# Optimization experiments

Measured on AMD Instinct MI355X. Metric: run time of the kernel, lower is better.

The kernel has to match this reference:

```python
import jax, jax.numpy as jnp
import numpy as np

VOCAB, EMB, B, L, H, OUT = 100000, 300, 2048, 200, 128, 20

def setup_inputs() -> dict:
    key = jax.random.key(0)
    ks = jax.random.split(key, 7)
    x = jax.random.randint(ks[0], (B, L), 0, VOCAB, dtype=jnp.int64 if jax.config.read('jax_enable_x64') else jnp.int32)
    lengths = jax.random.randint(ks[1], (B,), 1, L + 1, dtype=x.dtype)  # avoid zero length
    emb_table = jax.random.normal(ks[2], (VOCAB, EMB), dtype=jnp.float32)
    W1 = jax.random.normal(ks[3], (EMB, H), dtype=jnp.float32) * (1.0 / np.sqrt(EMB))
    b1 = jax.random.normal(ks[4], (H,), dtype=jnp.float32) * 0.01
    W2 = jax.random.normal(ks[5], (H, OUT), dtype=jnp.float32) * (1.0 / np.sqrt(H))
    b2 = jax.random.normal(ks[6], (OUT,), dtype=jnp.float32) * 0.01
    return {"x": x, "lengths": lengths, "emb_table": emb_table,
            "W1": W1, "b1": b1, "W2": W2, "b2": b2}

def reference(x, lengths, emb_table, W1, b1, W2, b2):
    # embedding lookup: [B, L, EMB]
    emb = emb_table[x]
    # faithful to original: sum over FULL sequence, divide by per-sample length
    rep = emb.sum(axis=1) / lengths.astype(emb.dtype)[:, None]  # [B, EMB]
    h = jax.nn.relu(rep @ W1 + b1)                              # [B, H]
    logits = h @ W2 + b2                                        # [B, OUT]
    return logits
```

## Files before the change

kernel.cpp:

```cpp
#include <hip/hip_runtime.h>

typedef _Float16 f16;
typedef _Float16 f16x8 __attribute__((ext_vector_type(8)));
typedef float    f32x4 __attribute__((ext_vector_type(4)));

#define VOCAB 100000
#define BB   2048
#define LL   200
#define EMB  300
#define HH   128
#define OUTD 20
#define NSRT 256
#define RPW  50

#define KPAD 320

__global__ void w1t_prep(const float* __restrict__ W1,
                         f16* __restrict__ w1t_hi,
                         f16* __restrict__ w1t_lo)
{
    const int n = blockIdx.x;
    const int k = threadIdx.x;
    const float v = (k < EMB) ? W1[(size_t)k * HH + n] : 0.f;
    const f16 hi = (f16)v;
    const f16 lo = (f16)(v - (float)hi);
    w1t_hi[(size_t)n * KPAD + k] = hi;
    w1t_lo[(size_t)n * KPAD + k] = lo;
}

#define BMp 128
#define BKp 32
#define KSTEPS 10

__global__ __launch_bounds__(256, 3) void proj_mfma(
    const float* __restrict__ table,
    const f16*   __restrict__ w1t_hi,
    const f16*   __restrict__ w1t_lo,
    f16*         __restrict__ P)
{
    __shared__ f16 Af_hi[8][64][8];
    __shared__ f16 Af_lo[8][64][8];
    __shared__ f16 Bf_hi[8][64][8];
    __shared__ f16 Bf_lo[8][64][8];

    const int t    = threadIdx.x;
    const int w    = t >> 6;
    const int lane = t & 63;
    const int row0 = blockIdx.x * BMp;

    f32x4 acc[2][8];
    #pragma unroll
    for (int i = 0; i < 2; ++i)
        #pragma unroll
        for (int j = 0; j < 8; ++j) acc[i][j] = (f32x4)0.f;

    for (int ks = 0; ks < KSTEPS; ++ks) {
        const int k0 = ks * BKp;

        #pragma unroll
        for (int half = 0; half < 2; ++half) {
            const int e  = t + 256 * half;
            const int mt = e >> 6;
            const int l  = e & 63;
            const int m  = (mt << 4) + (l & 15);
            const int kg = l >> 4;
            const int row = row0 + m;
            const int k   = k0 + kg * 8;
            const float* src = table + (size_t)row * EMB + k;
            float4 v0 = make_float4(0.f, 0.f, 0.f, 0.f);
            float4 v1 = make_float4(0.f, 0.f, 0.f, 0.f);
            if (row < VOCAB && k + 4 <= EMB) v0 = *(const float4*)(src);
            if (row < VOCAB && k + 8 <= EMB) v1 = *(const float4*)(src + 4);
            const float vv[8] = {v0.x, v0.y, v0.z, v0.w, v1.x, v1.y, v1.z, v1.w};
            f16x8 hi, lo;
            #pragma unroll
            for (int j = 0; j < 8; ++j) {
                const f16 h = (f16)vv[j];
                hi[j] = h;
                lo[j] = (f16)(vv[j] - (float)h);
            }
            *(f16x8*)&Af_hi[mt][l][0] = hi;
            *(f16x8*)&Af_lo[mt][l][0] = lo;
        }

        #pragma unroll
        for (int half = 0; half < 2; ++half) {
            const int e  = t + 256 * half;
            const int nt = e >> 6;
            const int l  = e & 63;
            const int n  = (nt << 4) + (l & 15);
            const int kg = l >> 4;
            const size_t off = (size_t)n * KPAD + k0 + kg * 8;
            *(f16x8*)&Bf_hi[nt][l][0] = *(const f16x8*)(w1t_hi + off);
            *(f16x8*)&Bf_lo[nt][l][0] = *(const f16x8*)(w1t_lo + off);
        }
        __syncthreads();

        f16x8 a_hi[2], a_lo[2];
        #pragma unroll
        for (int mt2 = 0; mt2 < 2; ++mt2) {
            a_hi[mt2] = *(const f16x8*)&Af_hi[2 * w + mt2][lane][0];
            a_lo[mt2] = *(const f16x8*)&Af_lo[2 * w + mt2][lane][0];
        }
        #pragma unroll
        for (int h = 0; h < 2; ++h) {
            f16x8 b_hi[4], b_lo[4];
            #pragma unroll
            for (int n4 = 0; n4 < 4; ++n4) {
                const int nt = h * 4 + n4;
                b_hi[n4] = *(const f16x8*)&Bf_hi[nt][lane][0];
                b_lo[n4] = *(const f16x8*)&Bf_lo[nt][lane][0];
            }
            #pragma unroll
            for (int mt2 = 0; mt2 < 2; ++mt2)
                #pragma unroll
                for (int n4 = 0; n4 < 4; ++n4) {
                    f32x4 c = acc[mt2][h * 4 + n4];
                    c = __builtin_amdgcn_mfma_f32_16x16x32_f16(a_hi[mt2], b_hi[n4], c, 0, 0, 0);
                    c = __builtin_amdgcn_mfma_f32_16x16x32_f16(a_hi[mt2], b_lo[n4], c, 0, 0, 0);
                    c = __builtin_amdgcn_mfma_f32_16x16x32_f16(a_lo[mt2], b_hi[n4], c, 0, 0, 0);
                    acc[mt2][h * 4 + n4] = c;
                }
        }
        __syncthreads();
    }

    #pragma unroll
    for (int mt2 = 0; mt2 < 2; ++mt2) {
        const int rbase = row0 + (2 * w + mt2) * 16 + 4 * (lane >> 4);
        #pragma unroll
        for (int nt = 0; nt < 8; ++nt) {
            const int col = nt * 16 + (lane & 15);
            const f32x4 v = acc[mt2][nt];
            #pragma unroll
            for (int j = 0; j < 4; ++j) {
                const int row = rbase + j;
                if (row < VOCAB)
                    P[(size_t)row * HH + col] = (f16)v[j];
            }
        }
    }
}

__global__ __launch_bounds__(256) void gather_mlp(
    const int*   __restrict__ x,
    const int*   __restrict__ lengths,
    const f16*   __restrict__ P,
    const float* __restrict__ b1,
    const float* __restrict__ W2,
    const float* __restrict__ b2,
    float*       __restrict__ out)
{
    __shared__ int   idx_s[NSRT];
    __shared__ float part_s[16][HH];
    __shared__ float h_s[HH];

    const int b    = blockIdx.x;
    const int t    = threadIdx.x;
    const int lane = t & 63;
    const int w    = t >> 6;

    idx_s[t] = (t < LL) ? x[b * LL + t] : 0x7FFFFFFF;
    __syncthreads();

    #pragma unroll
    for (int k = 2; k <= NSRT; k <<= 1) {
        #pragma unroll
        for (int j = k >> 1; j > 0; j >>= 1) {
            const int ixj = t ^ j;
            if (ixj > t) {
                const int a0 = idx_s[t];
                const int a1 = idx_s[ixj];
                const bool up = ((t & k) == 0);
                if ((a0 > a1) == up) { idx_s[t] = a1; idx_s[ixj] = a0; }
            }
            __syncthreads();
        }
    }

    const int myidx = (lane < RPW) ? idx_s[RPW * w + lane] : 0;

    const int c = lane & 15;
    const size_t coff = (size_t)c * 8;

    float acc[8];
    #pragma unroll
    for (int j = 0; j < 8; ++j) acc[j] = 0.f;

    #pragma unroll
    for (int i = 0; i < 12; ++i) {
        const int r0 = __builtin_amdgcn_readlane(myidx, 4 * i + 0);
        const int r1 = __builtin_amdgcn_readlane(myidx, 4 * i + 1);
        const int r2 = __builtin_amdgcn_readlane(myidx, 4 * i + 2);
        const int r3 = __builtin_amdgcn_readlane(myidx, 4 * i + 3);
        const int rlo  = (lane & 16) ? r1 : r0;
        const int rhi  = (lane & 16) ? r3 : r2;
        const int ridx = (lane & 32) ? rhi : rlo;
        const f16x8 v = *(const f16x8*)(P + (size_t)ridx * HH + coff);
        #pragma unroll
        for (int j = 0; j < 8; ++j) acc[j] += (float)v[j];
    }
    {
        const int r0 = __builtin_amdgcn_readlane(myidx, 48);
        const int r1 = __builtin_amdgcn_readlane(myidx, 49);
        const int ridx = (lane & 16) ? r1 : r0;
        const f16x8 v = *(const f16x8*)(P + (size_t)ridx * HH + coff);
        if (lane < 32) {
            #pragma unroll
            for (int j = 0; j < 8; ++j) acc[j] += (float)v[j];
        }
    }

    *(float4*)&part_s[t >> 4][c * 8]     = make_float4(acc[0], acc[1], acc[2], acc[3]);
    *(float4*)&part_s[t >> 4][c * 8 + 4] = make_float4(acc[4], acc[5], acc[6], acc[7]);
    __syncthreads();

    const float inv_len = 1.0f / (float)lengths[b];
    if (t < HH) {
        float s = 0.f;
        #pragma unroll
        for (int p = 0; p < 16; ++p) s += part_s[p][t];
        h_s[t] = fmaxf(fmaf(s, inv_len, b1[t]), 0.f);
    }
    __syncthreads();

    if (t < OUTD) {
        float o = b2[t];
        #pragma unroll
        for (int k = 0; k < HH; ++k)
            o = fmaf(h_s[k], W2[k * OUTD + t], o);
        out[b * OUTD + t] = o;
    }
}

__global__ __launch_bounds__(256) void fused_dnn(
    const int*   __restrict__ x,
    const int*   __restrict__ lengths,
    const float* __restrict__ table,
    const float* __restrict__ W1,
    const float* __restrict__ b1,
    const float* __restrict__ W2,
    const float* __restrict__ b2,
    float*       __restrict__ out)
{
    __shared__ int    idx_s[NSRT];
    __shared__ float4 part_s[4][76];
    __shared__ float  rep_s[EMB];
    __shared__ float  h_part[2][HH];
    __shared__ float  h_s[HH];

    const int b    = blockIdx.x;
    const int t    = threadIdx.x;
    const int w    = t >> 6;
    const int lane = t & 63;

    idx_s[t] = (t < LL) ? x[b * LL + t] : 0x7FFFFFFF;
    __syncthreads();

    #pragma unroll
    for (int k = 2; k <= NSRT; k <<= 1) {
        #pragma unroll
        for (int j = k >> 1; j > 0; j >>= 1) {
            const int ixj = t ^ j;
            if (ixj > t) {
                const int a0 = idx_s[t];
                const int a1 = idx_s[ixj];
                const bool up = ((t & k) == 0);
                if ((a0 > a1) == up) { idx_s[t] = a1; idx_s[ixj] = a0; }
            }
            __syncthreads();
        }
    }

    const int myidx = (lane < RPW) ? idx_s[w + 4 * lane] : 0;

    float4 acc_a = make_float4(0.f, 0.f, 0.f, 0.f);
    float4 acc_b = make_float4(0.f, 0.f, 0.f, 0.f);
    const bool hasb = (lane < (EMB / 4 - 64));

    #pragma unroll 5
    for (int i = 0; i < RPW; ++i) {
        const int ridx = __builtin_amdgcn_readlane(myidx, i);
        const float4* row = (const float4*)(table + (size_t)ridx * EMB);
        float4 va = row[lane];
        acc_a.x += va.x; acc_a.y += va.y; acc_a.z += va.z; acc_a.w += va.w;
        if (hasb) {
            float4 vb = row[64 + lane];
            acc_b.x += vb.x; acc_b.y += vb.y; acc_b.z += vb.z; acc_b.w += vb.w;
        }
    }

    part_s[w][lane] = acc_a;
    if (hasb) part_s[w][64 + lane] = acc_b;
    __syncthreads();

    const float inv_len = 1.0f / (float)lengths[b];
    const float* ps = (const float*)part_s;
    {
        float s = ps[t] + ps[304 + t] + ps[608 + t] + ps[912 + t];
        rep_s[t] = s * inv_len;
    }
    if (t < (EMB - 256)) {
        int c = 256 + t;
        float s = ps[c] + ps[304 + c] + ps[608 + c] + ps[912 + c];
        rep_s[c] = s * inv_len;
    }
    __syncthreads();

    {
        const int half = t >> 7;
        const int col  = t & 127;
        float hacc = (half == 0) ? b1[col] : 0.0f;
        const int k0 = half * (EMB / 2);
        #pragma unroll 5
        for (int k = k0; k < k0 + EMB / 2; ++k)
            hacc = fmaf(rep_s[k], W1[k * HH + col], hacc);
        h_part[half][col] = hacc;
    }
    __syncthreads();
    if (t < HH)
        h_s[t] = fmaxf(h_part[0][t] + h_part[1][t], 0.0f);
    __syncthreads();

    if (t < OUTD) {
        float oacc = b2[t];
        #pragma unroll
        for (int k = 0; k < HH; ++k)
            oacc = fmaf(h_s[k], W2[k * OUTD + t], oacc);
        out[b * OUTD + t] = oacc;
    }
}

extern "C" void kernel_launch(void* const* d_in, const int* in_sizes, int n_in,
                              void* d_out, int out_size, void* d_ws, size_t ws_size,
                              hipStream_t stream) {
    const int*   x       = (const int*)  d_in[0];
    const int*   lengths = (const int*)  d_in[1];
    const float* table   = (const float*)d_in[2];
    const float* W1      = (const float*)d_in[3];
    const float* b1      = (const float*)d_in[4];
    const float* W2      = (const float*)d_in[5];
    const float* b2      = (const float*)d_in[6];
    float*       out     = (float*)d_out;

    const size_t PELEMS  = (size_t)VOCAB * HH;
    const size_t W1TELEMS = (size_t)HH * KPAD;
    const size_t NEED = (PELEMS + 2 * W1TELEMS) * sizeof(f16);

    if (d_ws != nullptr && ws_size >= NEED) {
        f16* P      = (f16*)d_ws;
        f16* w1t_hi = P + PELEMS;
        f16* w1t_lo = w1t_hi + W1TELEMS;
        w1t_prep<<<HH, KPAD, 0, stream>>>(W1, w1t_hi, w1t_lo);
        const int mtiles = (VOCAB + BMp - 1) / BMp;
        proj_mfma<<<mtiles, 256, 0, stream>>>(table, w1t_hi, w1t_lo, P);
        gather_mlp<<<BB, 256, 0, stream>>>(x, lengths, P, b1, W2, b2, out);
    } else {
        fused_dnn<<<BB, 256, 0, stream>>>(x, lengths, table, W1, b1, W2, b2, out);
    }
}
```

Before: 248.0 us.

## Double-buffer projection GEMM, drop A lo-split, remove gather index sort

```diff
diff --git a/kernel.cpp b/kernel.cpp
--- a/kernel.cpp
+++ b/kernel.cpp
@@ -10,9 +10,7 @@
 #define EMB  300
 #define HH   128
 #define OUTD 20
-#define NSRT 256
 #define RPW  50
-
 #define KPAD 320
 
 __global__ void w1t_prep(const float* __restrict__ W1,
@@ -38,103 +36,103 @@
     const f16*   __restrict__ w1t_lo,
     f16*         __restrict__ P)
 {
-    __shared__ f16 Af_hi[8][64][8];
-    __shared__ f16 Af_lo[8][64][8];
-    __shared__ f16 Bf_hi[8][64][8];
-    __shared__ f16 Bf_lo[8][64][8];
+    __shared__ f16 Af[2][8][64][8];
 
     const int t    = threadIdx.x;
     const int w    = t >> 6;
     const int lane = t & 63;
     const int row0 = blockIdx.x * BMp;
 
-    f32x4 acc[2][8];
-    #pragma unroll
-    for (int i = 0; i < 2; ++i)
-        #pragma unroll
-        for (int j = 0; j < 8; ++j) acc[i][j] = (f32x4)0.f;
-
+    const int mtb = 4 * (w & 1);
+    const int ntb = 4 * (w >> 1);
+
+    const int sl    = t & 63;
+    const int skg   = (sl >> 4) * 8;
+    const int smt   = t >> 6;
+    const int srow0 = row0 + smt * 16 + (sl & 15);
+    const int srow1 = srow0 + 64;
+    const bool ok0  = (srow0 < VOCAB);
+    const bool ok1  = (srow1 < VOCAB);
+    const float* ap0 = table + (size_t)srow0 * EMB + skg;
+    const float* ap1 = table + (size_t)srow1 * EMB + skg;
+
+    const size_t boff = (size_t)(ntb * 16 + (lane & 15)) * KPAD + (lane >> 4) * 8;
+    const f16* bhp = w1t_hi + boff;
+    const f16* blp = w1t_lo + boff;
+
+    float4 sa0[2], sa1[2];
+
+    auto LOADA = [&](int k0) {
+        const int ka = k0 + skg;
+        const float4 z = make_float4(0.f, 0.f, 0.f, 0.f);
+        sa0[0] = (ok0 && ka + 4 <= EMB) ? *(const float4*)(ap0 + k0)     : z;
+        sa0[1] = (ok0 && ka + 8 <= EMB) ? *(const float4*)(ap0 + k0 + 4) : z;
+        sa1[0] = (ok1 && ka + 4 <= EMB) ? *(const float4*)(ap1 + k0)     : z;
+        sa1[1] = (ok1 && ka + 8 <= EMB) ? *(const float4*)(ap1 + k0 + 4) : z;
+    };
+    auto CVTWRITE = [&](int buf) {
+        const float v0[8] = {sa0[0].x, sa0[0].y, sa0[0].z, sa0[0].w,
+                             sa0[1].x, sa0[1].y, sa0[1].z, sa0[1].w};
+        const float v1[8] = {sa1[0].x, sa1[0].y, sa1[0].z, sa1[0].w,
+                             sa1[1].x, sa1[1].y, sa1[1].z, sa1[1].w};
+        f16x8 h0, h1;
+        #pragma unroll
+        for (int j = 0; j < 8; ++j) { h0[j] = (f16)v0[j]; h1[j] = (f16)v1[j]; }
+        *(f16x8*)&Af[buf][smt][sl][0]     = h0;
+        *(f16x8*)&Af[buf][smt + 4][sl][0] = h1;
+    };
+
+    f32x4 acc[4][4];
+    #pragma unroll
+    for (int i = 0; i < 4; ++i)
+        #pragma unroll
+        for (int j = 0; j < 4; ++j) acc[i][j] = (f32x4)0.f;
+
+    LOADA(0);
+    CVTWRITE(0);
+    __syncthreads();
+
+    int cur = 0;
     for (int ks = 0; ks < KSTEPS; ++ks) {
         const int k0 = ks * BKp;
 
-        #pragma unroll
-        for (int half = 0; half < 2; ++half) {
-            const int e  = t + 256 * half;
-            const int mt = e >> 6;
-            const int l  = e & 63;
-            const int m  = (mt << 4) + (l & 15);
-            const int kg = l >> 4;
-            const int row = row0 + m;
-            const int k   = k0 + kg * 8;
-            const float* src = table + (size_t)row * EMB + k;
-            float4 v0 = make_float4(0.f, 0.f, 0.f, 0.f);
-            float4 v1 = make_float4(0.f, 0.f, 0.f, 0.f);
-            if (row < VOCAB && k + 4 <= EMB) v0 = *(const float4*)(src);
-            if (row < VOCAB && k + 8 <= EMB) v1 = *(const float4*)(src + 4);
-            const float vv[8] = {v0.x, v0.y, v0.z, v0.w, v1.x, v1.y, v1.z, v1.w};
-            f16x8 hi, lo;
+        f16x8 bh[4], bl[4];
+        #pragma unroll
+        for (int n4 = 0; n4 < 4; ++n4) {
+            bh[n4] = *(const f16x8*)(bhp + (size_t)n4 * 16 * KPAD + k0);
+            bl[n4] = *(const f16x8*)(blp + (size_t)n4 * 16 * KPAD + k0);
+        }
+
+        if (ks + 1 < KSTEPS) LOADA(k0 + BKp);
+
+        f16x8 a[4];
+        #pragma unroll
+        for (int m4 = 0; m4 < 4; ++m4)
+            a[m4] = *(const f16x8*)&Af[cur][mtb + m4][lane][0];
+
+        #pragma unroll
+        for (int n4 = 0; n4 < 4; ++n4)
             #pragma unroll
-            for (int j = 0; j < 8; ++j) {
-                const f16 h = (f16)vv[j];
-                hi[j] = h;
-                lo[j] = (f16)(vv[j] - (float)h);
+            for (int m4 = 0; m4 < 4; ++m4) {
+                acc[m4][n4] = __builtin_amdgcn_mfma_f32_16x16x32_f16(a[m4], bh[n4], acc[m4][n4], 0, 0, 0);
+                acc[m4][n4] = __builtin_amdgcn_mfma_f32_16x16x32_f16(a[m4], bl[n4], acc[m4][n4], 0, 0, 0);
             }
-            *(f16x8*)&Af_hi[mt][l][0] = hi;
-            *(f16x8*)&Af_lo[mt][l][0] = lo;
-        }
-
-        #pragma unroll
-        for (int half = 0; half < 2; ++half) {
-            const int e  = t + 256 * half;
-            const int nt = e >> 6;
-            const int l  = e & 63;
-            const int n  = (nt << 4) + (l & 15);
-            const int kg = l >> 4;
-            const size_t off = (size_t)n * KPAD + k0 + kg * 8;
-            *(f16x8*)&Bf_hi[nt][l][0] = *(const f16x8*)(w1t_hi + off);
-            *(f16x8*)&Bf_lo[nt][l][0] = *(const f16x8*)(w1t_lo + off);
-        }
+
+        if (ks + 1 < KSTEPS) CVTWRITE(cur ^ 1);
         __syncthreads();
-
-        f16x8 a_hi[2], a_lo[2];
-        #pragma unroll
-        for (int mt2 = 0; mt2 < 2; ++mt2) {
-            a_hi[mt2] = *(const f16x8*)&Af_hi[2 * w + mt2][lane][0];
-            a_lo[mt2] = *(const f16x8*)&Af_lo[2 * w + mt2][lane][0];
-        }
-        #pragma unroll
-        for (int h = 0; h < 2; ++h) {
-            f16x8 b_hi[4], b_lo[4];
-            #pragma unroll
-            for (int n4 = 0; n4 < 4; ++n4) {
-                const int nt = h * 4 + n4;
-                b_hi[n4] = *(const f16x8*)&Bf_hi[nt][lane][0];
-                b_lo[n4] = *(const f16x8*)&Bf_lo[nt][lane][0];
-            }
-            #pragma unroll
-            for (int mt2 = 0; mt2 < 2; ++mt2)
-                #pragma unroll
-                for (int n4 = 0; n4 < 4; ++n4) {
-                    f32x4 c = acc[mt2][h * 4 + n4];
-                    c = __builtin_amdgcn_mfma_f32_16x16x32_f16(a_hi[mt2], b_hi[n4], c, 0, 0, 0);
-                    c = __builtin_amdgcn_mfma_f32_16x16x32_f16(a_hi[mt2], b_lo[n4], c, 0, 0, 0);
-                    c = __builtin_amdgcn_mfma_f32_16x16x32_f16(a_lo[mt2], b_hi[n4], c, 0, 0, 0);
-                    acc[mt2][h * 4 + n4] = c;
-                }
-        }
-        __syncthreads();
-    }
-
-    #pragma unroll
-    for (int mt2 = 0; mt2 < 2; ++mt2) {
-        const int rbase = row0 + (2 * w + mt2) * 16 + 4 * (lane >> 4);
-        #pragma unroll
-        for (int nt = 0; nt < 8; ++nt) {
-            const int col = nt * 16 + (lane & 15);
-            const f32x4 v = acc[mt2][nt];
+        cur ^= 1;
+    }
+
+    #pragma unroll
+    for (int m4 = 0; m4 < 4; ++m4) {
+        const int rb = row0 + (mtb + m4) * 16 + 4 * (lane >> 4);
+        #pragma unroll
+        for (int n4 = 0; n4 < 4; ++n4) {
+            const int col = (ntb + n4) * 16 + (lane & 15);
+            const f32x4 v = acc[m4][n4];
             #pragma unroll
             for (int j = 0; j < 4; ++j) {
-                const int row = rbase + j;
+                const int row = rb + j;
                 if (row < VOCAB)
                     P[(size_t)row * HH + col] = (f16)v[j];
             }
@@ -151,7 +149,6 @@
     const float* __restrict__ b2,
     float*       __restrict__ out)
 {
-    __shared__ int   idx_s[NSRT];
     __shared__ float part_s[16][HH];
     __shared__ float h_s[HH];
 
@@ -160,25 +157,7 @@
     const int lane = t & 63;
     const int w    = t >> 6;
 
-    idx_s[t] = (t < LL) ? x[b * LL + t] : 0x7FFFFFFF;
-    __syncthreads();
-
-    #pragma unroll
-    for (int k = 2; k <= NSRT; k <<= 1) {
-        #pragma unroll
-        for (int j = k >> 1; j > 0; j >>= 1) {
-            const int ixj = t ^ j;
-            if (ixj > t) {
-                const int a0 = idx_s[t];
-                const int a1 = idx_s[ixj];
-                const bool up = ((t & k) == 0);
-                if ((a0 > a1) == up) { idx_s[t] = a1; idx_s[ixj] = a0; }
-            }
-            __syncthreads();
-        }
-    }
-
-    const int myidx = (lane < RPW) ? idx_s[RPW * w + lane] : 0;
+    const int myidx = (lane < RPW) ? x[b * LL + RPW * w + lane] : 0;
 
     const int c = lane & 15;
     const size_t coff = (size_t)c * 8;
@@ -233,6 +212,7 @@
     }
 }
 
+#define NSRT 256
 __global__ __launch_bounds__(256) void fused_dnn(
     const int*   __restrict__ x,
     const int*   __restrict__ lengths,
@@ -343,7 +323,7 @@
     const float* b2      = (const float*)d_in[6];
     float*       out     = (float*)d_out;
 
-    const size_t PELEMS  = (size_t)VOCAB * HH;
+    const size_t PELEMS   = (size_t)VOCAB * HH;
     const size_t W1TELEMS = (size_t)HH * KPAD;
     const size_t NEED = (PELEMS + 2 * W1TELEMS) * sizeof(f16);
 
```

Result: slower. 306.8 us (+23.7%).
